# Kernel optimization log

Measured on AMD Instinct MI355X. Metric: run time of the kernel, lower is better.

The kernel has to match this reference:

```python
import jax, jax.numpy as jnp
import numpy as np

B = 8192
D = 1024
NUM_CLASSES = 128
EPS = 1e-8  # torch F.cosine_similarity default eps


def setup_inputs() -> dict:
    key = jax.random.key(0)
    k1, k2, k3 = jax.random.split(key, 3)
    label_tensor = jax.random.randint(k1, (B,), 0, NUM_CLASSES, dtype=jnp.int64 if jax.config.jax_enable_x64 else jnp.int32)
    feature_a = jax.random.normal(k2, (B, D), dtype=jnp.float32)
    feature_b = jax.random.normal(k3, (B, D), dtype=jnp.float32)
    return {"label_tensor": label_tensor, "feature_a": feature_a, "feature_b": feature_b}


def reference(label_tensor, feature_a, feature_b):
    # Pairwise cosine similarity: cos_score[i, k] = cos(a_i, b_k), shape [B, B]
    dots = feature_a @ feature_b.T  # [B, B]
    na = jnp.linalg.norm(feature_a, axis=1)  # [B]
    nb = jnp.linalg.norm(feature_b, axis=1)  # [B]
    cos_score = dots / jnp.maximum(na[:, None] * nb[None, :], EPS)
    # Row-softmax (torch softmax dim=1 on the [B, B] matrix)
    logp = jax.nn.log_softmax(cos_score, axis=1)
    # Label-equality mask: positives for row i are all j with same label
    mask = (label_tensor[:, None] == label_tensor[None, :]).astype(cos_score.dtype)  # [B, B]
    per_row = -(mask * logp).sum(axis=1) / mask.sum(axis=1)  # diagonal guarantees >=1 positive
    loss = per_row.mean()
    return loss, cos_score
```

## Files before the change

kernel.cpp:

```cpp
#include <hip/hip_runtime.h>
#include <hip/hip_bf16.h>

#define NB 8192
#define ND 1024

typedef __bf16 bf16x8 __attribute__((ext_vector_type(8)));
typedef int    i32x4  __attribute__((ext_vector_type(4)));
typedef float  f32x4  __attribute__((ext_vector_type(4)));

__device__ inline void gload_lds16(const void* g, void* l) {
    __builtin_amdgcn_global_load_lds(
        (const __attribute__((address_space(1))) unsigned int*)g,
        (__attribute__((address_space(3))) unsigned int*)l,
        16, 0, 0);
}

__device__ inline void bload(const unsigned short* p, i32x4& d) {
    asm volatile("global_load_dwordx4 %0, %1, off"
                 : "=v"(d) : "v"(p) : "memory");
}

__device__ inline unsigned short f2bf(float x) {
    unsigned int u = __float_as_uint(x);
    return (unsigned short)((u + 0x7fffu + ((u >> 16) & 1u)) >> 16);
}

#define BARRIER() asm volatile("s_barrier" ::: "memory")
#define VMCNT6()  asm volatile("s_waitcnt vmcnt(6)" ::: "memory")
#define VMCNT0()  asm volatile("s_waitcnt vmcnt(0)" ::: "memory")
#define LGKM0()   asm volatile("s_waitcnt lgkmcnt(0)" ::: "memory")

__global__ __launch_bounds__(256) void prep_kernel(
    const float* __restrict__ A, const float* __restrict__ Bm,
    unsigned short* __restrict__ wa, unsigned short* __restrict__ wb2,
    float* __restrict__ na, float* __restrict__ nb)
{
    int b = blockIdx.x;
    int wid = threadIdx.x >> 6, lane = threadIdx.x & 63;
    bool isA = (b < 2048);
    int row = (isA ? b : b - 2048) * 4 + wid;
    const float* rp = (isA ? A : Bm) + (size_t)row * ND;

    float ss = 0.f;
#pragma unroll
    for (int t = 0; t < 4; ++t) {
        int c = lane * 4 + t * 256;
        float4 v = *reinterpret_cast<const float4*>(rp + c);
        ss += v.x * v.x + v.y * v.y + v.z * v.z + v.w * v.w;
        ushort4 u;
        u.x = f2bf(v.x); u.y = f2bf(v.y); u.z = f2bf(v.z); u.w = f2bf(v.w);
        if (isA) {
            *reinterpret_cast<ushort4*>(wa + (size_t)row * ND + c) = u;
        } else {
            size_t idx = (size_t)(row >> 4) * 16384 + (c >> 3) * 128
                       + (row & 15) * 8 + (c & 7);
            *reinterpret_cast<ushort4*>(wb2 + idx) = u;
        }
    }
#pragma unroll
    for (int off = 32; off; off >>= 1) ss += __shfl_xor(ss, off);
    if (lane == 0) (isA ? na : nb)[row] = sqrtf(ss);
}

__global__ __launch_bounds__(256) void hist_kernel(
    const int* __restrict__ labels, int* __restrict__ hist)
{
    __shared__ int h[128];
    int tid = threadIdx.x;
    if (tid < 128) h[tid] = 0;
    __syncthreads();
    for (int i = tid; i < NB; i += 256) atomicAdd(&h[labels[i]], 1);
    __syncthreads();
    if (tid < 128) hist[tid] = h[tid];
}

__global__ __launch_bounds__(256) void gemm_cos(
    const unsigned short* __restrict__ wa, const unsigned short* __restrict__ wb2,
    const float* __restrict__ na, const float* __restrict__ nb,
    const int* __restrict__ labels,
    float* __restrict__ C, float* __restrict__ pe, float* __restrict__ pm)
{
    __shared__ unsigned short lds[12288];

    const int bid = blockIdx.x;
    const int tm  = (bid & 7) * 8 + ((bid >> 3) & 7);
    const int tn  = bid >> 6;

    const int tid  = threadIdx.x;
    const int lane = tid & 63;
    const int wid  = tid >> 6;
    const int wr   = wid >> 1, wc = wid & 1;
    const int l15  = lane & 15, lg = lane >> 4;

    const int m0 = tm * 128, n0 = tn * 128;

    const int srow = tid >> 2;
    const int sg   = (tid & 3) ^ ((tid >> 3) & 3);
    const unsigned short* pA0 = wa + (size_t)(m0 + srow) * ND + sg * 8;
    const unsigned short* pA1 = pA0 + 64 * ND;
    const int stW = wid * 512;

    const int kg  = (lg ^ ((lane >> 1) & 3)) * 8;
    const int rdA = wr * 2048 + l15 * 32 + kg;

    const unsigned short* qB = wb2 + (size_t)tn * 131072 + wc * 65536
                             + lg * 128 + l15 * 8;

    f32x4 acc[4][4];
#pragma unroll
    for (int i = 0; i < 4; ++i)
#pragma unroll
        for (int j = 0; j < 4; ++j) acc[i][j] = (f32x4){0.f, 0.f, 0.f, 0.f};

    i32x4 breg[2][4];

#define STAGE_A(t, BUF) do { \
    gload_lds16(pA0 + (t) * 32, &lds[(BUF) + stW]); \
    gload_lds16(pA1 + (t) * 32, &lds[(BUF) + 2048 + stW]); } while (0)

#define BLOAD(t, P) do { _Pragma("unroll") \
    for (int n_ = 0; n_ < 4; ++n_) \
        bload(qB + (t) * 512 + n_ * 16384, breg[P][n_]); } while (0)

    STAGE_A(0, 0);
    STAGE_A(1, 4096);
    BLOAD(0, 0);
    VMCNT6();
    BARRIER();

#pragma unroll
    for (int t = 0; t < 32; ++t) {
        const int cb  = (t % 3) * 4096;
        const int nb2 = ((t + 2) % 3) * 4096;
        const int cp  = t & 1, np = cp ^ 1;
        if (t < 30) STAGE_A(t + 2, nb2);
        if (t < 31) BLOAD(t + 1, np);
        bf16x8 af[4];
#pragma unroll
        for (int m_ = 0; m_ < 4; ++m_)
            af[m_] = *reinterpret_cast<const bf16x8*>(&lds[cb + rdA + m_ * 512]);
        if (t < 31) VMCNT6();
        else        VMCNT0();
        __builtin_amdgcn_sched_barrier(0);
#pragma unroll
        for (int m_ = 0; m_ < 4; ++m_)
#pragma unroll
            for (int n_ = 0; n_ < 4; ++n_)
                acc[m_][n_] = __builtin_amdgcn_mfma_f32_16x16x32_bf16(
                    af[m_], __builtin_bit_cast(bf16x8, breg[cp][n_]),
                    acc[m_][n_], 0, 0, 0);
        LGKM0();
        BARRIER();
    }

#undef BLOAD
#undef STAGE_A

    __syncthreads();
    float* pl = reinterpret_cast<float*>(lds);

    float nbv[4]; int labc[4];
#pragma unroll
    for (int n = 0; n < 4; ++n) {
        int c = n0 + wc * 64 + n * 16 + l15;
        nbv[n] = nb[c]; labc[n] = labels[c];
    }

#pragma unroll
    for (int m = 0; m < 4; ++m) {
#pragma unroll
        for (int jj = 0; jj < 4; ++jj) {
            int rl = wr * 64 + m * 16 + lg * 4 + jj;
            int r  = m0 + rl;
            float nav = na[r]; int labr = labels[r];
            float es = 0.f, ms = 0.f;
#pragma unroll
            for (int n = 0; n < 4; ++n) {
                int c = n0 + wc * 64 + n * 16 + l15;
                float v = acc[m][n][jj] / fmaxf(nav * nbv[n], 1e-8f);
                C[(size_t)r * NB + c] = v;
                es += __expf(v);
                ms += (labc[n] == labr) ? v : 0.f;
            }
#pragma unroll
            for (int off = 1; off < 16; off <<= 1) {
                es += __shfl_xor(es, off);
                ms += __shfl_xor(ms, off);
            }
            if (l15 == 0) {
                int o = rl * 4 + wc * 2;
                pl[o] = es; pl[o + 1] = ms;
            }
        }
    }
    __syncthreads();
    if (tid < 128) {
        float es = pl[tid * 4]     + pl[tid * 4 + 2];
        float ms = pl[tid * 4 + 1] + pl[tid * 4 + 3];
        pe[tn * NB + m0 + tid] = es;
        pm[tn * NB + m0 + tid] = ms;
    }
}

__global__ __launch_bounds__(256) void loss_final(
    const float* __restrict__ pe, const float* __restrict__ pm,
    const int* __restrict__ labels, const int* __restrict__ hist,
    float* __restrict__ per_row)
{
    int row = blockIdx.x * 256 + threadIdx.x;
    float es = 0.f, ms = 0.f;
#pragma unroll
    for (int t = 0; t < 64; ++t) {
        es += pe[t * NB + row];
        ms += pm[t * NB + row];
    }
    per_row[row] = logf(es) - ms / (float)hist[labels[row]];
}

__global__ __launch_bounds__(256) void finalize(
    const float* __restrict__ per_row, float* __restrict__ out)
{
    __shared__ float sm[256];
    float s = 0.f;
    for (int i = threadIdx.x; i < NB; i += 256) s += per_row[i];
    sm[threadIdx.x] = s;
    __syncthreads();
    for (int k = 128; k; k >>= 1) {
        if (threadIdx.x < k) sm[threadIdx.x] += sm[threadIdx.x + k];
        __syncthreads();
    }
    if (threadIdx.x == 0) out[0] = sm[0] * (1.0f / (float)NB);
}

extern "C" void kernel_launch(void* const* d_in, const int* in_sizes, int n_in,
                              void* d_out, int out_size, void* d_ws, size_t ws_size,
                              hipStream_t stream) {
    const int*   labels = (const int*)d_in[0];
    const float* A      = (const float*)d_in[1];
    const float* Bm     = (const float*)d_in[2];
    float* out = (float*)d_out;

    char* ws = (char*)d_ws;
    unsigned short* wa  = (unsigned short*)(ws);
    unsigned short* wb2 = (unsigned short*)(ws + 16777216);
    float* na      = (float*)(ws + 33554432);
    float* nb      = (float*)(ws + 33554432 + 32768);
    float* per_row = (float*)(ws + 33554432 + 65536);
    int*   hist    = (int*)  (ws + 33554432 + 98304);
    float* pe      = (float*)(ws + 33554432 + 131072);
    float* pm      = (float*)(ws + 33554432 + 131072 + 2097152);

    float* cosm = out + 1;

    prep_kernel<<<4096, 256, 0, stream>>>(A, Bm, wa, wb2, na, nb);
    hist_kernel<<<1,    256, 0, stream>>>(labels, hist);
    gemm_cos   <<<4096, 256, 0, stream>>>(wa, wb2, na, nb, labels, cosm, pe, pm);
    loss_final <<<32,   256, 0, stream>>>(pe, pm, labels, hist, per_row);
    finalize   <<<1,    256, 0, stream>>>(per_row, out);
}
```

Before: 295.4 us.

## Replace LDS-staged 128x128 GEMM with single-wave 64x64 register-only tiles

```diff
diff --git a/kernel.cpp b/kernel.cpp
--- a/kernel.cpp
+++ b/kernel.cpp
@@ -5,41 +5,31 @@
 #define ND 1024
 
 typedef __bf16 bf16x8 __attribute__((ext_vector_type(8)));
-typedef int    i32x4  __attribute__((ext_vector_type(4)));
 typedef float  f32x4  __attribute__((ext_vector_type(4)));
-
-__device__ inline void gload_lds16(const void* g, void* l) {
-    __builtin_amdgcn_global_load_lds(
-        (const __attribute__((address_space(1))) unsigned int*)g,
-        (__attribute__((address_space(3))) unsigned int*)l,
-        16, 0, 0);
-}
-
-__device__ inline void bload(const unsigned short* p, i32x4& d) {
-    asm volatile("global_load_dwordx4 %0, %1, off"
-                 : "=v"(d) : "v"(p) : "memory");
-}
 
 __device__ inline unsigned short f2bf(float x) {
     unsigned int u = __float_as_uint(x);
     return (unsigned short)((u + 0x7fffu + ((u >> 16) & 1u)) >> 16);
 }
 
-#define BARRIER() asm volatile("s_barrier" ::: "memory")
-#define VMCNT6()  asm volatile("s_waitcnt vmcnt(6)" ::: "memory")
-#define VMCNT0()  asm volatile("s_waitcnt vmcnt(0)" ::: "memory")
-#define LGKM0()   asm volatile("s_waitcnt lgkmcnt(0)" ::: "memory")
+__device__ inline float bf2f(unsigned short u) {
+    unsigned int v = ((unsigned int)u) << 16;
+    return __uint_as_float(v);
+}
 
 __global__ __launch_bounds__(256) void prep_kernel(
     const float* __restrict__ A, const float* __restrict__ Bm,
-    unsigned short* __restrict__ wa, unsigned short* __restrict__ wb2,
+    unsigned short* __restrict__ wa2, unsigned short* __restrict__ wb2,
     float* __restrict__ na, float* __restrict__ nb)
 {
     int b = blockIdx.x;
     int wid = threadIdx.x >> 6, lane = threadIdx.x & 63;
     bool isA = (b < 2048);
     int row = (isA ? b : b - 2048) * 4 + wid;
-    const float* rp = (isA ? A : Bm) + (size_t)row * ND;
+    const float*    rp  = (isA ? A : Bm) + (size_t)row * ND;
+    unsigned short* dst = (isA ? wa2 : wb2);
+
+    const size_t rbase = (size_t)(row >> 4) * 16384 + (row & 15) * 8;
 
     float ss = 0.f;
 #pragma unroll
@@ -49,13 +39,8 @@
         ss += v.x * v.x + v.y * v.y + v.z * v.z + v.w * v.w;
         ushort4 u;
         u.x = f2bf(v.x); u.y = f2bf(v.y); u.z = f2bf(v.z); u.w = f2bf(v.w);
-        if (isA) {
-            *reinterpret_cast<ushort4*>(wa + (size_t)row * ND + c) = u;
-        } else {
-            size_t idx = (size_t)(row >> 4) * 16384 + (c >> 3) * 128
-                       + (row & 15) * 8 + (c & 7);
-            *reinterpret_cast<ushort4*>(wb2 + idx) = u;
-        }
+        size_t idx = rbase + (size_t)(c >> 3) * 128 + (c & 7);
+        *reinterpret_cast<ushort4*>(dst + idx) = u;
     }
 #pragma unroll
     for (int off = 32; off; off >>= 1) ss += __shfl_xor(ss, off);
@@ -74,37 +59,29 @@
     if (tid < 128) hist[tid] = h[tid];
 }
 
-__global__ __launch_bounds__(256) void gemm_cos(
-    const unsigned short* __restrict__ wa, const unsigned short* __restrict__ wb2,
+__global__ __launch_bounds__(64, 3) void gemm_cos(
+    const unsigned short* __restrict__ wa2, const unsigned short* __restrict__ wb2,
     const float* __restrict__ na, const float* __restrict__ nb,
     const int* __restrict__ labels,
-    float* __restrict__ C, float* __restrict__ pe, float* __restrict__ pm)
-{
-    __shared__ unsigned short lds[12288];
-
+    float* __restrict__ C,
+    unsigned short* __restrict__ pe, unsigned short* __restrict__ pm)
+{
     const int bid = blockIdx.x;
-    const int tm  = (bid & 7) * 8 + ((bid >> 3) & 7);
-    const int tn  = bid >> 6;
-
-    const int tid  = threadIdx.x;
-    const int lane = tid & 63;
-    const int wid  = tid >> 6;
-    const int wr   = wid >> 1, wc = wid & 1;
+    const int tm  = (bid & 7) * 16 + ((bid >> 3) & 15);
+    const int tn  = bid >> 7;
+
+    const int lane = threadIdx.x & 63;
     const int l15  = lane & 15, lg = lane >> 4;
 
-    const int m0 = tm * 128, n0 = tn * 128;
-
-    const int srow = tid >> 2;
-    const int sg   = (tid & 3) ^ ((tid >> 3) & 3);
-    const unsigned short* pA0 = wa + (size_t)(m0 + srow) * ND + sg * 8;
-    const unsigned short* pA1 = pA0 + 64 * ND;
-    const int stW = wid * 512;
-
-    const int kg  = (lg ^ ((lane >> 1) & 3)) * 8;
-    const int rdA = wr * 2048 + l15 * 32 + kg;
-
-    const unsigned short* qB = wb2 + (size_t)tn * 131072 + wc * 65536
-                             + lg * 128 + l15 * 8;
+    const int m0 = tm * 64, n0 = tn * 64;
+
+    const unsigned short* pa[4];
+    const unsigned short* pb[4];
+#pragma unroll
+    for (int m = 0; m < 4; ++m) {
+        pa[m] = wa2 + (size_t)(tm * 4 + m) * 16384 + lg * 128 + l15 * 8;
+        pb[m] = wb2 + (size_t)(tn * 4 + m) * 16384 + lg * 128 + l15 * 8;
+    }
 
     f32x4 acc[4][4];
 #pragma unroll
@@ -112,57 +89,35 @@
 #pragma unroll
         for (int j = 0; j < 4; ++j) acc[i][j] = (f32x4){0.f, 0.f, 0.f, 0.f};
 
-    i32x4 breg[2][4];
-
-#define STAGE_A(t, BUF) do { \
-    gload_lds16(pA0 + (t) * 32, &lds[(BUF) + stW]); \
-    gload_lds16(pA1 + (t) * 32, &lds[(BUF) + 2048 + stW]); } while (0)
-
-#define BLOAD(t, P) do { _Pragma("unroll") \
-    for (int n_ = 0; n_ < 4; ++n_) \
-        bload(qB + (t) * 512 + n_ * 16384, breg[P][n_]); } while (0)
-
-    STAGE_A(0, 0);
-    STAGE_A(1, 4096);
-    BLOAD(0, 0);
-    VMCNT6();
-    BARRIER();
+    bf16x8 a[2][4], b[2][4];
+#pragma unroll
+    for (int m = 0; m < 4; ++m) {
+        a[0][m] = *reinterpret_cast<const bf16x8*>(pa[m]);
+        b[0][m] = *reinterpret_cast<const bf16x8*>(pb[m]);
+    }
 
 #pragma unroll
     for (int t = 0; t < 32; ++t) {
-        const int cb  = (t % 3) * 4096;
-        const int nb2 = ((t + 2) % 3) * 4096;
-        const int cp  = t & 1, np = cp ^ 1;
-        if (t < 30) STAGE_A(t + 2, nb2);
-        if (t < 31) BLOAD(t + 1, np);
-        bf16x8 af[4];
-#pragma unroll
-        for (int m_ = 0; m_ < 4; ++m_)
-            af[m_] = *reinterpret_cast<const bf16x8*>(&lds[cb + rdA + m_ * 512]);
-        if (t < 31) VMCNT6();
-        else        VMCNT0();
-        __builtin_amdgcn_sched_barrier(0);
-#pragma unroll
-        for (int m_ = 0; m_ < 4; ++m_)
-#pragma unroll
-            for (int n_ = 0; n_ < 4; ++n_)
-                acc[m_][n_] = __builtin_amdgcn_mfma_f32_16x16x32_bf16(
-                    af[m_], __builtin_bit_cast(bf16x8, breg[cp][n_]),
-                    acc[m_][n_], 0, 0, 0);
-        LGKM0();
-        BARRIER();
-    }
-
-#undef BLOAD
-#undef STAGE_A
-
-    __syncthreads();
-    float* pl = reinterpret_cast<float*>(lds);
+        const int cur = t & 1, nxt = cur ^ 1;
+        if (t < 31) {
+#pragma unroll
+            for (int m = 0; m < 4; ++m) {
+                a[nxt][m] = *reinterpret_cast<const bf16x8*>(pa[m] + (t + 1) * 512);
+                b[nxt][m] = *reinterpret_cast<const bf16x8*>(pb[m] + (t + 1) * 512);
+            }
+        }
+#pragma unroll
+        for (int m = 0; m < 4; ++m)
+#pragma unroll
+            for (int n = 0; n < 4; ++n)
+                acc[m][n] = __builtin_amdgcn_mfma_f32_16x16x32_bf16(
+                    a[cur][m], b[cur][n], acc[m][n], 0, 0, 0);
+    }
 
     float nbv[4]; int labc[4];
 #pragma unroll
     for (int n = 0; n < 4; ++n) {
-        int c = n0 + wc * 64 + n * 16 + l15;
+        int c = n0 + n * 16 + l15;
         nbv[n] = nb[c]; labc[n] = labels[c];
     }
 
@@ -170,13 +125,12 @@
     for (int m = 0; m < 4; ++m) {
 #pragma unroll
         for (int jj = 0; jj < 4; ++jj) {
-            int rl = wr * 64 + m * 16 + lg * 4 + jj;
-            int r  = m0 + rl;
+            int r = m0 + m * 16 + lg * 4 + jj;
             float nav = na[r]; int labr = labels[r];
             float es = 0.f, ms = 0.f;
 #pragma unroll
             for (int n = 0; n < 4; ++n) {
-                int c = n0 + wc * 64 + n * 16 + l15;
+                int c = n0 + n * 16 + l15;
                 float v = acc[m][n][jj] / fmaxf(nav * nbv[n], 1e-8f);
                 C[(size_t)r * NB + c] = v;
                 es += __expf(v);
@@ -188,31 +142,24 @@
                 ms += __shfl_xor(ms, off);
             }
             if (l15 == 0) {
-                int o = rl * 4 + wc * 2;
-                pl[o] = es; pl[o + 1] = ms;
+                pe[tn * NB + r] = f2bf(es);
+                pm[tn * NB + r] = f2bf(ms);
             }
         }
     }
-    __syncthreads();
-    if (tid < 128) {
-        float es = pl[tid * 4]     + pl[tid * 4 + 2];
-        float ms = pl[tid * 4 + 1] + pl[tid * 4 + 3];
-        pe[tn * NB + m0 + tid] = es;
-        pm[tn * NB + m0 + tid] = ms;
-    }
 }
 
 __global__ __launch_bounds__(256) void loss_final(
-    const float* __restrict__ pe, const float* __restrict__ pm,
+    const unsigned short* __restrict__ pe, const unsigned short* __restrict__ pm,
     const int* __restrict__ labels, const int* __restrict__ hist,
     float* __restrict__ per_row)
 {
     int row = blockIdx.x * 256 + threadIdx.x;
     float es = 0.f, ms = 0.f;
 #pragma unroll
-    for (int t = 0; t < 64; ++t) {
-        es += pe[t * NB + row];
-        ms += pm[t * NB + row];
+    for (int t = 0; t < 128; ++t) {
+        es += bf2f(pe[t * NB + row]);
+        ms += bf2f(pm[t * NB + row]);
     }
     per_row[row] = logf(es) - ms / (float)hist[labels[row]];
 }
@@ -241,20 +188,20 @@
     float* out = (float*)d_out;
 
     char* ws = (char*)d_ws;
-    unsigned short* wa  = (unsigned short*)(ws);
+    unsigned short* wa2 = (unsigned short*)(ws);
     unsigned short* wb2 = (unsigned short*)(ws + 16777216);
     float* na      = (float*)(ws + 33554432);
     float* nb      = (float*)(ws + 33554432 + 32768);
     float* per_row = (float*)(ws + 33554432 + 65536);
     int*   hist    = (int*)  (ws + 33554432 + 98304);
-    float* pe      = (float*)(ws + 33554432 + 131072);
-    float* pm      = (float*)(ws + 33554432 + 131072 + 2097152);
+    unsigned short* pe = (unsigned short*)(ws + 33554432 + 131072);
+    unsigned short* pm = (unsigned short*)(ws + 33554432 + 131072 + 2097152);
 
     float* cosm = out + 1;
 
-    prep_kernel<<<4096, 256, 0, stream>>>(A, Bm, wa, wb2, na, nb);
-    hist_kernel<<<1,    256, 0, stream>>>(labels, hist);
-    gemm_cos   <<<4096, 256, 0, stream>>>(wa, wb2, na, nb, labels, cosm, pe, pm);
-    loss_final <<<32,   256, 0, stream>>>(pe, pm, labels, hist, per_row);
-    finalize   <<<1,    256, 0, stream>>>(per_row, out);
-}
+    prep_kernel<<<4096,  256, 0, stream>>>(A, Bm, wa2, wb2, na, nb);
+    hist_kernel<<<1,     256, 0, stream>>>(labels, hist);
+    gemm_cos   <<<16384,  64, 0, stream>>>(wa2, wb2, na, nb, labels, cosm, pe, pm);
+    loss_final <<<32,    256, 0, stream>>>(pe, pm, labels, hist, per_row);
+    finalize   <<<1,     256, 0, stream>>>(per_row, out);
+}
```

After: 304.9 us. 3.2% more time.
